# Kernel optimization log

Hardware: AMD Instinct MI355X
Metric: run time of the kernel (lower is better)

## Reference

```python
import jax, jax.numpy as jnp
import numpy as np
import math

C_IN, C_OUT = 256, 256
KH, KW = 3, 3
STRIDE, PAD = 1, 1
CURV = 1.0
SQRT_C = math.sqrt(CURV)
EPS = 1e-15

def _beta(a, b):
    return math.exp(math.lgamma(a) + math.lgamma(b) - math.lgamma(a + b))

BETA_NI = _beta(C_IN / 2.0, 0.5)                 # beta(n_i/2, 1/2)
BETA_N = _beta(C_IN * KH * KW / 2.0, 0.5)        # beta(n/2, 1/2)


def logmap0(y, axis):
    n = jnp.maximum(jnp.linalg.norm(y, axis=axis, keepdims=True), EPS)
    return jnp.arctanh(jnp.minimum(SQRT_C * n, 1.0 - 1e-7)) * y / (SQRT_C * n)


def expmap0(v, axis):
    n = jnp.maximum(jnp.linalg.norm(v, axis=axis, keepdims=True), EPS)
    return jnp.tanh(SQRT_C * n) * v / (SQRT_C * n)


def unfold(x):
    # torch.nn.Unfold: x [B,C,H,W] -> [B, C*KH*KW, L], channel-major patch order
    B, C, H, W = x.shape
    Ho = (H + 2 * PAD - KH) // STRIDE + 1
    Wo = (W + 2 * PAD - KW) // STRIDE + 1
    xp = jnp.pad(x, ((0, 0), (0, 0), (PAD, PAD), (PAD, PAD)))
    cols = [xp[:, :, i:i + STRIDE * Ho:STRIDE, j:j + STRIDE * Wo:STRIDE]
            for i in range(KH) for j in range(KW)]
    patches = jnp.stack(cols, axis=2)            # [B, C, KH*KW, Ho, Wo]
    return patches.reshape(B, C * KH * KW, Ho * Wo), Ho, Wo


def poincare_fc(x, z, r):
    # x: [..., D_in] on ball, z: [D_in, D_out], r: [D_out]
    x2 = jnp.sum(x * x, axis=-1, keepdims=True)
    lam = 2.0 / (1.0 - CURV * x2)                # conformal factor lambda_x
    z_norm = jnp.maximum(jnp.linalg.norm(z, axis=0), EPS)  # [D_out]
    xz = x @ z                                   # [..., D_out]
    two_csr = 2.0 * SQRT_C * r
    inner = (SQRT_C * lam * xz / z_norm * jnp.cosh(two_csr)
             - (lam - 1.0) * jnp.sinh(two_csr))
    v = 2.0 * z_norm / SQRT_C * jnp.arcsinh(inner)   # hyperplane distances
    w = jnp.sinh(SQRT_C * v) / SQRT_C
    return w / (1.0 + jnp.sqrt(1.0 + CURV * jnp.sum(w * w, axis=-1, keepdims=True)))


def setup_inputs() -> dict:
    key = jax.random.key(0)
    k1, k2, k3 = jax.random.split(key, 3)
    # tangent vectors -> points on the Poincare ball (man_dim=1)
    v = 0.05 * jax.random.normal(k1, (16, C_IN, 64, 64), dtype=jnp.float32)
    x = expmap0(v, axis=1)
    std = (2.0 * C_IN * KH * KW * C_OUT) ** (-0.5)
    weights = std * jax.random.normal(k2, (KH * KW * C_IN, C_OUT), dtype=jnp.float32)
    bias = 0.01 * jax.random.normal(k3, (C_OUT,), dtype=jnp.float32)
    return {"x": x, "weights": weights, "bias": bias}


def reference(x, weights, bias):
    B = x.shape[0]
    v = logmap0(x, axis=1) * (BETA_N / BETA_NI)      # log map + beta scaling
    u, Ho, Wo = unfold(v)                            # [B, CK, L]
    u = jnp.swapaxes(u, 1, 2)                        # [B, L, CK]
    p = expmap0(u, axis=-1)                          # back onto the ball
    y = poincare_fc(p, weights, bias)                # [B, L, C_OUT]
    return jnp.swapaxes(y, 1, 2).reshape(B, C_OUT, Ho, Wo)
```

## Files before the change

kernel.cpp:

```cpp
#include <hip/hip_runtime.h>
#include <cmath>

typedef __bf16 bf16;
typedef __bf16 bf16x8 __attribute__((ext_vector_type(8)));
typedef float f32x4 __attribute__((ext_vector_type(4)));

#define SBAR() __builtin_amdgcn_sched_barrier(0)


__device__ inline void gload16(const void* g, void* l) {
    __builtin_amdgcn_global_load_lds(
        (const __attribute__((address_space(1))) unsigned int*)g,
        (__attribute__((address_space(3))) unsigned int*)l, 16, 0, 0);
}

__global__ void k_prep_zt(const float* __restrict__ z, bf16* __restrict__ zt6) {
    int s = blockIdx.x;
    int cc = s / 9, tap = s % 9;
    int co = threadIdx.x;
#pragma unroll
    for (int g = 0; g < 4; ++g) {
        bf16x8 pk;
#pragma unroll
        for (int e = 0; e < 8; ++e) {
            int c = cc * 32 + g * 8 + e;
            pk[e] = (bf16)z[(size_t)(c * 9 + tap) * 256 + co];
        }
        *(bf16x8*)(zt6 + ((size_t)(s * 256 + co) * 4 + g) * 8) = pk;
    }
}

__global__ void k_prep_cols(const float* __restrict__ z, const float* __restrict__ r,
                            float* __restrict__ zn, float* __restrict__ ch,
                            float* __restrict__ sh) {
    __shared__ float red[256];
    int co = blockIdx.x, t = threadIdx.x;
    float s = 0.f;
    for (int i = 0; i < 9; ++i) {
        float v = z[(size_t)(i * 256 + t) * 256 + co];
        s += v * v;
    }
    red[t] = s;
    __syncthreads();
    for (int off = 128; off >= 1; off >>= 1) {
        if (t < off) red[t] += red[t + off];
        __syncthreads();
    }
    if (t == 0) {
        zn[co] = fmaxf(sqrtf(red[0]), 1e-15f);
        float tc = 2.f * r[co];
        ch[co] = coshf(tc);
        sh[co] = sinhf(tc);
    }
}

__global__ void k_logmap(const float* __restrict__ x, unsigned int* __restrict__ vt_u,
                         float* __restrict__ sq, float Rbeta) {
    __shared__ float tile[256][33];
    __shared__ float red[8][32];
    __shared__ float afac[32];
    int tid = threadIdx.x;
    int blk = blockIdx.x;
    int b = blk >> 7;
    int pix0 = (blk & 127) << 5;

    for (int it = 0; it < 32; ++it) {
        int c = it * 8 + (tid >> 5);
        int p = tid & 31;
        tile[c][p] = x[((size_t)b * 256 + c) * 4096 + pix0 + p];
    }
    __syncthreads();

    {
        int part = tid >> 5, p = tid & 31;
        float s = 0.f;
        for (int i = 0; i < 32; ++i) {
            float v = tile[part * 32 + i][p];
            s += v * v;
        }
        red[part][p] = s;
    }
    __syncthreads();
    if (tid < 32) {
        float n2 = 0.f;
        for (int i = 0; i < 8; ++i) n2 += red[i][tid];
        float n = sqrtf(n2);
        float nc = fmaxf(n, 1e-15f);
        float a = atanhf(fminf(nc, 0.9999999f)) / nc * Rbeta;
        afac[tid] = a;
        sq[(size_t)b * 4096 + pix0 + tid] = a * a * n2;
    }
    __syncthreads();

    for (int it = 0; it < 16; ++it) {
        int idx = it * 256 + tid;
        int p = idx >> 7;
        int cp = idx & 127;
        float a = afac[p];
        float v0 = a * tile[2 * cp][p];
        float v1 = a * tile[2 * cp + 1][p];
        union { bf16 h[2]; unsigned int u; } pk;
        pk.h[0] = (bf16)v0;
        pk.h[1] = (bf16)v1;
        vt_u[((size_t)b * 4096 + pix0 + p) * 128 + cp] = pk.u;
    }
}

__global__ void k_boxsum(const float* __restrict__ sq, float* __restrict__ nusq) {
    int idx = blockIdx.x * 256 + threadIdx.x;
    int b = idx >> 12, hw = idx & 4095, h = hw >> 6, w = hw & 63;
    const float* s = sq + ((size_t)b << 12);
    float acc = 0.f;
    for (int dh = -1; dh <= 1; ++dh) {
        int hh = h + dh;
        if ((unsigned)hh >= 64u) continue;
        for (int dw = -1; dw <= 1; ++dw) {
            int ww = w + dw;
            if ((unsigned)ww >= 64u) continue;
            acc += s[hh * 64 + ww];
        }
    }
    nusq[idx] = acc;
}

__global__ void
__attribute__((amdgpu_flat_work_group_size(512, 512)))
__attribute__((amdgpu_waves_per_eu(4, 4)))
k_hconv(const bf16* __restrict__ vt, const bf16* __restrict__ zt6,
        const float* __restrict__ nusq,
        const float* __restrict__ znp, const float* __restrict__ chp,
        const float* __restrict__ shp, float* __restrict__ out) {
    __shared__ __align__(1024) char Asb[16896];
    __shared__ float s_lds[128], lam_lds[128];
    __shared__ float red[128][4];

    int tid = threadIdx.x;
    int bid = blockIdx.x;
    int bh = ((bid & 7) << 6) | (bid >> 3);
    int b = bh >> 5, h0 = (bh & 31) << 1;

    if (tid < 32) {
        int u = tid >> 1, side = tid & 1;
        *(f32x4*)(Asb + u * 1056 + side * 1040) = (f32x4){0.f, 0.f, 0.f, 0.f};
    }

    if (tid >= 128 && tid < 256) {
        int t = tid - 128;
        int h = h0 + (t >> 6), w = t & 63;
        float q = nusq[((size_t)b << 12) + h * 64 + w];
        float ncl = fmaxf(sqrtf(q), 1e-15f);
        float p = __expf(2.f * ncl);
        float tt = (p - 1.f) / (p + 1.f);
        s_lds[t] = tt / ncl;
        lam_lds[t] = 2.f / (1.f - tt * tt);
    }

    int wave = tid >> 6, lane = tid & 63;
    int wn = wave & 3, wm = wave >> 2;
    int lrow = lane & 15, lk = lane >> 4;

    f32x4 acc[4][4];
#pragma unroll
    for (int m = 0; m < 4; ++m)
#pragma unroll
        for (int n = 0; n < 4; ++n) acc[m][n] = (f32x4){0.f, 0.f, 0.f, 0.f};

    const bf16* vb = vt + (((size_t)b) << 12) * 256;

    auto stageA = [&](int ccn) {
#pragma unroll
        for (int it = 0; it < 2; ++it) {
            int u = wave * 2 + it;
            int r = u >> 2, g = u & 3;
            int hr = h0 - 1 + r;
            hr = hr < 0 ? 0 : (hr > 63 ? 63 : hr);
            const bf16* gp = vb + ((size_t)(hr * 64 + lane)) * 256 + ccn * 32 + g * 8;
            gload16(gp, Asb + u * 1056 + 16);
        }
    };

    const bf16* bp = zt6 + ((size_t)(wn * 64 + lrow) * 4 + lk) * 8;
    bf16x8 bA[4], bB[4];
#pragma unroll
    for (int n = 0; n < 4; ++n) bA[n] = *(const bf16x8*)(bp + n * 512);
    const bf16* bnp = bp + 8192;

    stageA(0);
    __syncthreads();
    SBAR();

    const char* ApB = Asb + lk * 1056 + lrow * 16;

#define STAGE(CCV, TAP, CUR, NXT)                                            \
    {                                                                        \
        const int s_ = (CCV) * 9 + (TAP);                                    \
        if (s_ < 71) {                                                       \
            NXT[0] = *(const bf16x8*)(bnp);                                  \
            NXT[1] = *(const bf16x8*)(bnp + 512);                            \
            NXT[2] = *(const bf16x8*)(bnp + 1024);                           \
            NXT[3] = *(const bf16x8*)(bnp + 1536);                           \
            bnp += 8192;                                                     \
        }                                                                    \
        if ((TAP) == 0) {                                                    \
            SBAR();                                                          \
            asm volatile("s_waitcnt vmcnt(4)" ::: "memory");                 \
            SBAR();                                                          \
            asm volatile("s_barrier" ::: "memory");         \
            SBAR();                                                          \
        }                                                                    \
        {                                                                    \
            const int dh_ = (TAP) / 3 - 1, dw_ = (TAP) % 3 - 1;              \
            int hh_ = h0 + wm + dh_;                                         \
            if ((unsigned)hh_ < 64u) {                                       \
                const char* Ap_ = ApB + (wm + dh_ + 1) * 4224 + (dw_ + 1) * 16; \
                bf16x8 a0 = *(const bf16x8*)(Ap_);                           \
                bf16x8 a1 = *(const bf16x8*)(Ap_ + 256);                     \
                bf16x8 a2 = *(const bf16x8*)(Ap_ + 512);                     \
                bf16x8 a3 = *(const bf16x8*)(Ap_ + 768);                     \
                __builtin_amdgcn_s_setprio(1);                               \
                acc[0][0] = __builtin_amdgcn_mfma_f32_16x16x32_bf16(a0, CUR[0], acc[0][0], 0, 0, 0); \
                acc[1][0] = __builtin_amdgcn_mfma_f32_16x16x32_bf16(a1, CUR[0], acc[1][0], 0, 0, 0); \
                acc[2][0] = __builtin_amdgcn_mfma_f32_16x16x32_bf16(a2, CUR[0], acc[2][0], 0, 0, 0); \
                acc[3][0] = __builtin_amdgcn_mfma_f32_16x16x32_bf16(a3, CUR[0], acc[3][0], 0, 0, 0); \
                acc[0][1] = __builtin_amdgcn_mfma_f32_16x16x32_bf16(a0, CUR[1], acc[0][1], 0, 0, 0); \
                acc[1][1] = __builtin_amdgcn_mfma_f32_16x16x32_bf16(a1, CUR[1], acc[1][1], 0, 0, 0); \
                acc[2][1] = __builtin_amdgcn_mfma_f32_16x16x32_bf16(a2, CUR[1], acc[2][1], 0, 0, 0); \
                acc[3][1] = __builtin_amdgcn_mfma_f32_16x16x32_bf16(a3, CUR[1], acc[3][1], 0, 0, 0); \
                acc[0][2] = __builtin_amdgcn_mfma_f32_16x16x32_bf16(a0, CUR[2], acc[0][2], 0, 0, 0); \
                acc[1][2] = __builtin_amdgcn_mfma_f32_16x16x32_bf16(a1, CUR[2], acc[1][2], 0, 0, 0); \
                acc[2][2] = __builtin_amdgcn_mfma_f32_16x16x32_bf16(a2, CUR[2], acc[2][2], 0, 0, 0); \
                acc[3][2] = __builtin_amdgcn_mfma_f32_16x16x32_bf16(a3, CUR[2], acc[3][2], 0, 0, 0); \
                acc[0][3] = __builtin_amdgcn_mfma_f32_16x16x32_bf16(a0, CUR[3], acc[0][3], 0, 0, 0); \
                acc[1][3] = __builtin_amdgcn_mfma_f32_16x16x32_bf16(a1, CUR[3], acc[1][3], 0, 0, 0); \
                acc[2][3] = __builtin_amdgcn_mfma_f32_16x16x32_bf16(a2, CUR[3], acc[2][3], 0, 0, 0); \
                acc[3][3] = __builtin_amdgcn_mfma_f32_16x16x32_bf16(a3, CUR[3], acc[3][3], 0, 0, 0); \
                __builtin_amdgcn_s_setprio(0);                               \
            }                                                                \
        }                                                                    \
        if ((TAP) == 8 && (CCV) < 7) {                                       \
            SBAR();                                                          \
            asm volatile("s_barrier" ::: "memory");    \
            SBAR();                                                          \
            stageA((CCV) + 1);                                               \
            SBAR();                                                          \
        }                                                                    \
    }

#pragma unroll 1
    for (int cc2 = 0; cc2 < 4; ++cc2) {
        const int c0 = cc2 * 2, c1 = c0 + 1;
        STAGE(c0, 0, bA, bB) STAGE(c0, 1, bB, bA) STAGE(c0, 2, bA, bB)
        STAGE(c0, 3, bB, bA) STAGE(c0, 4, bA, bB) STAGE(c0, 5, bB, bA)
        STAGE(c0, 6, bA, bB) STAGE(c0, 7, bB, bA) STAGE(c0, 8, bA, bB)
        STAGE(c1, 0, bB, bA) STAGE(c1, 1, bA, bB) STAGE(c1, 2, bB, bA)
        STAGE(c1, 3, bA, bB) STAGE(c1, 4, bB, bA) STAGE(c1, 5, bA, bB)
        STAGE(c1, 6, bB, bA) STAGE(c1, 7, bA, bB) STAGE(c1, 8, bB, bA)
    }
#undef STAGE

    float cz[4], sh4[4], tz[4];
#pragma unroll
    for (int n = 0; n < 4; ++n) {
        int co = wn * 64 + n * 16 + lrow;
        float zn = znp[co];
        cz[n] = chp[co] / zn;
        sh4[n] = shp[co];
        tz[n] = 2.f * zn;
    }

#pragma unroll
    for (int m = 0; m < 4; ++m) {
#pragma unroll
        for (int r = 0; r < 4; ++r) {
            int wp = wm * 64 + m * 16 + 4 * lk + r;
            float s = s_lds[wp], lam = lam_lds[wp];
            float lm1 = lam - 1.f;
            float psum = 0.f;
#pragma unroll
            for (int n = 0; n < 4; ++n) {
                float xz = s * acc[m][n][r];
                float inner = lam * xz * cz[n] - lm1 * sh4[n];
                float as = __logf(inner + sqrtf(inner * inner + 1.f));
                float p = __expf(tz[n] * as);
                float w = 0.5f * (p - __builtin_amdgcn_rcpf(p));
                acc[m][n][r] = w;
                psum += w * w;
            }
            psum += __shfl_xor(psum, 1);
            psum += __shfl_xor(psum, 2);
            psum += __shfl_xor(psum, 4);
            psum += __shfl_xor(psum, 8);
            if (lrow == 0) red[wp][wn] = psum;
        }
    }
    __syncthreads();

    float dinv[4][4];
#pragma unroll
    for (int m = 0; m < 4; ++m)
#pragma unroll
        for (int r = 0; r < 4; ++r) {
            int wp = wm * 64 + m * 16 + 4 * lk + r;
            float tot = (red[wp][0] + red[wp][1]) + (red[wp][2] + red[wp][3]);
            dinv[m][r] = __builtin_amdgcn_rcpf(1.f + sqrtf(1.f + tot));
        }

    float* ob = out + (size_t)b * 256 * 4096 + (h0 + wm) * 64;
#pragma unroll
    for (int m = 0; m < 4; ++m) {
#pragma unroll
        for (int n = 0; n < 4; ++n) {
            int co = wn * 64 + n * 16 + lrow;
            f32x4 o;
#pragma unroll
            for (int r = 0; r < 4; ++r) o[r] = acc[m][n][r] * dinv[m][r];
            *(f32x4*)(ob + (size_t)co * 4096 + m * 16 + 4 * lk) = o;
        }
    }
}

extern "C" void kernel_launch(void* const* d_in, const int* in_sizes, int n_in,
                              void* d_out, int out_size, void* d_ws, size_t ws_size,
                              hipStream_t stream) {
    const float* x = (const float*)d_in[0];
    const float* z = (const float*)d_in[1];
    const float* r = (const float*)d_in[2];
    float* out = (float*)d_out;

    char* ws = (char*)d_ws;
    bf16* vt = (bf16*)ws;
    float* sq = (float*)(ws + 33554432);
    float* nusq = (float*)(ws + 33816576);
    bf16* zt6 = (bf16*)(ws + 34078720);
    float* zn = (float*)(ws + 35258368);
    float* ch = (float*)(ws + 35259392);
    float* sh = (float*)(ws + 35260416);
    if (ws_size < 35261440) return;

    double bni = lgamma(128.0) + lgamma(0.5) - lgamma(128.5);
    double bn = lgamma(1152.0) + lgamma(0.5) - lgamma(1152.5);
    float Rbeta = (float)exp(bn - bni);

    k_prep_zt<<<72, 256, 0, stream>>>(z, zt6);
    k_prep_cols<<<256, 256, 0, stream>>>(z, r, zn, ch, sh);
    k_logmap<<<2048, 256, 0, stream>>>(x, (unsigned int*)vt, sq, Rbeta);
    k_boxsum<<<256, 256, 0, stream>>>(sq, nusq);
    k_hconv<<<512, 512, 0, stream>>>(vt, zt6, nusq, zn, ch, sh, out);
}
```

Measured before the change: 138.4 us.

## Fuse 3x3 norm box-sum into conv kernel and shrink tile to one row

Removes the separate box-sum kernel and its intermediate buffer. The conv kernel now computes each pixel's 3x3 squared-norm sum directly from the per-pixel squared norms. Each block now handles a single output row with 256 threads (4 waves) instead of two rows with 512 threads, and the grid doubles to 1024 blocks. This saves a launch and a global round-trip and gives more, smaller blocks for scheduling. In exchange, halo reuse drops: each block stages 3 input rows per output row instead of 4 rows per 2 output rows, so there is more load traffic per output.

```diff
diff --git a/kernel.cpp b/kernel.cpp
--- a/kernel.cpp
+++ b/kernel.cpp
@@ -106,57 +106,51 @@
     }
 }
 
-__global__ void k_boxsum(const float* __restrict__ sq, float* __restrict__ nusq) {
-    int idx = blockIdx.x * 256 + threadIdx.x;
-    int b = idx >> 12, hw = idx & 4095, h = hw >> 6, w = hw & 63;
-    const float* s = sq + ((size_t)b << 12);
-    float acc = 0.f;
-    for (int dh = -1; dh <= 1; ++dh) {
-        int hh = h + dh;
-        if ((unsigned)hh >= 64u) continue;
-        for (int dw = -1; dw <= 1; ++dw) {
-            int ww = w + dw;
-            if ((unsigned)ww >= 64u) continue;
-            acc += s[hh * 64 + ww];
-        }
-    }
-    nusq[idx] = acc;
-}
-
 __global__ void
-__attribute__((amdgpu_flat_work_group_size(512, 512)))
-__attribute__((amdgpu_waves_per_eu(4, 4)))
+__attribute__((amdgpu_flat_work_group_size(256, 256)))
+__attribute__((amdgpu_waves_per_eu(3)))
 k_hconv(const bf16* __restrict__ vt, const bf16* __restrict__ zt6,
-        const float* __restrict__ nusq,
+        const float* __restrict__ sq,
         const float* __restrict__ znp, const float* __restrict__ chp,
         const float* __restrict__ shp, float* __restrict__ out) {
-    __shared__ __align__(1024) char Asb[16896];
-    __shared__ float s_lds[128], lam_lds[128];
-    __shared__ float red[128][4];
+    __shared__ __align__(1024) char Asb[12672];
+    __shared__ float s_lds[64], lam_lds[64];
+    __shared__ float red[64][4];
 
     int tid = threadIdx.x;
     int bid = blockIdx.x;
-    int bh = ((bid & 7) << 6) | (bid >> 3);
-    int b = bh >> 5, h0 = (bh & 31) << 1;
-
-    if (tid < 32) {
+    int bh = ((bid & 7) << 7) | (bid >> 3);
+    int b = bh >> 6, h = bh & 63;
+
+    if (tid < 24) {
         int u = tid >> 1, side = tid & 1;
         *(f32x4*)(Asb + u * 1056 + side * 1040) = (f32x4){0.f, 0.f, 0.f, 0.f};
     }
 
-    if (tid >= 128 && tid < 256) {
-        int t = tid - 128;
-        int h = h0 + (t >> 6), w = t & 63;
-        float q = nusq[((size_t)b << 12) + h * 64 + w];
+    if (tid >= 64 && tid < 128) {
+        int w = tid - 64;
+        const float* sb = sq + ((size_t)b << 12);
+        float q = 0.f;
+#pragma unroll
+        for (int dh = -1; dh <= 1; ++dh) {
+            int hhh = h + dh;
+            if ((unsigned)hhh >= 64u) continue;
+#pragma unroll
+            for (int dw = -1; dw <= 1; ++dw) {
+                int ww = w + dw;
+                if ((unsigned)ww >= 64u) continue;
+                q += sb[hhh * 64 + ww];
+            }
+        }
         float ncl = fmaxf(sqrtf(q), 1e-15f);
         float p = __expf(2.f * ncl);
         float tt = (p - 1.f) / (p + 1.f);
-        s_lds[t] = tt / ncl;
-        lam_lds[t] = 2.f / (1.f - tt * tt);
+        s_lds[w] = tt / ncl;
+        lam_lds[w] = 2.f / (1.f - tt * tt);
     }
 
     int wave = tid >> 6, lane = tid & 63;
-    int wn = wave & 3, wm = wave >> 2;
+    int wn = wave;
     int lrow = lane & 15, lk = lane >> 4;
 
     f32x4 acc[4][4];
@@ -169,10 +163,10 @@
 
     auto stageA = [&](int ccn) {
 #pragma unroll
-        for (int it = 0; it < 2; ++it) {
-            int u = wave * 2 + it;
+        for (int it = 0; it < 3; ++it) {
+            int u = wave * 3 + it;
             int r = u >> 2, g = u & 3;
-            int hr = h0 - 1 + r;
+            int hr = h - 1 + r;
             hr = hr < 0 ? 0 : (hr > 63 ? 63 : hr);
             const bf16* gp = vb + ((size_t)(hr * 64 + lane)) * 256 + ccn * 32 + g * 8;
             gload16(gp, Asb + u * 1056 + 16);
@@ -201,18 +195,18 @@
             NXT[3] = *(const bf16x8*)(bnp + 1536);                           \
             bnp += 8192;                                                     \
         }                                                                    \
-        if ((TAP) == 0) {                                                    \
-            SBAR();                                                          \
-            asm volatile("s_waitcnt vmcnt(4)" ::: "memory");                 \
+        if ((TAP) == 0 && (CCV) > 0) {                                       \
+            SBAR();                                                          \
+            asm volatile("s_waitcnt vmcnt(4)" ::: "memory");   \
             SBAR();                                                          \
             asm volatile("s_barrier" ::: "memory");         \
             SBAR();                                                          \
         }                                                                    \
         {                                                                    \
             const int dh_ = (TAP) / 3 - 1, dw_ = (TAP) % 3 - 1;              \
-            int hh_ = h0 + wm + dh_;                                         \
+            int hh_ = h + dh_;                                               \
             if ((unsigned)hh_ < 64u) {                                       \
-                const char* Ap_ = ApB + (wm + dh_ + 1) * 4224 + (dw_ + 1) * 16; \
+                const char* Ap_ = ApB + (dh_ + 1) * 4224 + (dw_ + 1) * 16;   \
                 bf16x8 a0 = *(const bf16x8*)(Ap_);                           \
                 bf16x8 a1 = *(const bf16x8*)(Ap_ + 256);                     \
                 bf16x8 a2 = *(const bf16x8*)(Ap_ + 512);                     \
@@ -248,7 +242,7 @@
 
 #pragma unroll 1
     for (int cc2 = 0; cc2 < 4; ++cc2) {
-        const int c0 = cc2 * 2, c1 = c0 + 1;
+        const int c0 = 2 * cc2, c1 = c0 + 1;
         STAGE(c0, 0, bA, bB) STAGE(c0, 1, bB, bA) STAGE(c0, 2, bA, bB)
         STAGE(c0, 3, bB, bA) STAGE(c0, 4, bA, bB) STAGE(c0, 5, bB, bA)
         STAGE(c0, 6, bA, bB) STAGE(c0, 7, bB, bA) STAGE(c0, 8, bA, bB)
@@ -272,7 +266,7 @@
     for (int m = 0; m < 4; ++m) {
 #pragma unroll
         for (int r = 0; r < 4; ++r) {
-            int wp = wm * 64 + m * 16 + 4 * lk + r;
+            int wp = m * 16 + 4 * lk + r;
             float s = s_lds[wp], lam = lam_lds[wp];
             float lm1 = lam - 1.f;
             float psum = 0.f;
@@ -300,12 +294,12 @@
     for (int m = 0; m < 4; ++m)
 #pragma unroll
         for (int r = 0; r < 4; ++r) {
-            int wp = wm * 64 + m * 16 + 4 * lk + r;
+            int wp = m * 16 + 4 * lk + r;
             float tot = (red[wp][0] + red[wp][1]) + (red[wp][2] + red[wp][3]);
             dinv[m][r] = __builtin_amdgcn_rcpf(1.f + sqrtf(1.f + tot));
         }
 
-    float* ob = out + (size_t)b * 256 * 4096 + (h0 + wm) * 64;
+    float* ob = out + (size_t)b * 256 * 4096 + h * 64;
 #pragma unroll
     for (int m = 0; m < 4; ++m) {
 #pragma unroll
@@ -330,7 +324,6 @@
     char* ws = (char*)d_ws;
     bf16* vt = (bf16*)ws;
     float* sq = (float*)(ws + 33554432);
-    float* nusq = (float*)(ws + 33816576);
     bf16* zt6 = (bf16*)(ws + 34078720);
     float* zn = (float*)(ws + 35258368);
     float* ch = (float*)(ws + 35259392);
@@ -344,6 +337,5 @@
     k_prep_zt<<<72, 256, 0, stream>>>(z, zt6);
     k_prep_cols<<<256, 256, 0, stream>>>(z, r, zn, ch, sh);
     k_logmap<<<2048, 256, 0, stream>>>(x, (unsigned int*)vt, sq, Rbeta);
-    k_boxsum<<<256, 256, 0, stream>>>(sq, nusq);
-    k_hconv<<<512, 512, 0, stream>>>(vt, zt6, nusq, zn, ch, sh, out);
-}
+    k_hconv<<<1024, 256, 0, stream>>>(vt, zt6, sq, zn, ch, sh, out);
+}
```

Measured after the change: 138.6 us. No clear change (+0.2%).
